# Kernel tuning notes

Hardware: AMD Instinct MI355X
Metric: run time of the kernel (lower is better)

Reference implementation:

```python
import jax, jax.numpy as jnp
import numpy as np

N_NODES = 10000
IN_DIM, EDGE_DIM, HID_DIM, OUT_DIM = 128, 64, 256, 128
N_EDGES = 640000


def setup_inputs() -> dict:
    key = jax.random.key(0)
    ks = jax.random.split(key, 8)
    x = jax.random.normal(ks[0], (N_NODES, IN_DIM), dtype=jnp.float32)
    edge_index = jax.random.randint(ks[1], (2, N_EDGES), 0, N_NODES, dtype=jnp.int64)
    edge_attr = jax.random.normal(ks[2], (N_EDGES, EDGE_DIM), dtype=jnp.float32)
    # MLP params (PyTorch Linear: y = x @ W.T + b), Kaiming-uniform-ish scale
    s1 = 1.0 / np.sqrt(IN_DIM + EDGE_DIM)
    s2 = 1.0 / np.sqrt(HID_DIM)
    W1 = jax.random.uniform(ks[3], (HID_DIM, IN_DIM + EDGE_DIM), minval=-s1, maxval=s1, dtype=jnp.float32)
    b1 = jax.random.uniform(ks[4], (HID_DIM,), minval=-s1, maxval=s1, dtype=jnp.float32)
    W2 = jax.random.uniform(ks[5], (OUT_DIM, HID_DIM), minval=-s2, maxval=s2, dtype=jnp.float32)
    b2 = jax.random.uniform(ks[6], (OUT_DIM,), minval=-s2, maxval=s2, dtype=jnp.float32)
    return {"x": x, "edge_index": edge_index, "edge_attr": edge_attr,
            "W1": W1, "b1": b1, "W2": W2, "b2": b2}


def reference(x, edge_index, edge_attr, W1, b1, W2, b2):
    # GINE-style concat-message conv: gather -> per-edge MLP -> scatter-add.
    src = edge_index[0]  # message source node x_j
    dst = edge_index[1]  # aggregation target node
    m = jnp.concatenate([x[src], edge_attr], axis=-1)         # [E, F+Fe]
    h = jax.nn.relu(m @ W1.T + b1)                            # [E, H]
    msg = h @ W2.T + b2                                       # [E, O]
    out = jax.ops.segment_sum(msg, dst, num_segments=x.shape[0])  # [N, O]
    return out
```

## Files before the change

### kernel.cpp

```cpp
#include <hip/hip_runtime.h>

#define N_NODES 10000
#define IN_DIM 128
#define EDGE_DIM 64
#define HID_DIM 256
#define OUT_DIM 128
#define N_EDGES 640000


typedef __bf16 bf16x8 __attribute__((ext_vector_type(8)));
typedef float f32x4 __attribute__((ext_vector_type(4)));

static __device__ __forceinline__ unsigned pk_pre(float lo, float hi) {
    return (__builtin_bit_cast(unsigned, lo) >> 16) |
           (__builtin_bit_cast(unsigned, hi) & 0xFFFF0000u);
}
static __device__ __forceinline__ unsigned short f2bf(float f) {
    unsigned u = __builtin_bit_cast(unsigned, f);
    u = (u + 0x7fffu + ((u >> 16) & 1u)) >> 16;
    return (unsigned short)u;
}

__global__ void zero_kernel(float* __restrict__ out) {
    int t = blockIdx.x * 256 + threadIdx.x;
    if (t < 320000) ((float4*)out)[t] = make_float4(0.f, 0.f, 0.f, 0.f);
}

#define FENCE_LGKM()  asm volatile("s_waitcnt lgkmcnt(0)" ::: "memory")
#define SCHED_FENCE() __builtin_amdgcn_sched_barrier(0)

__global__ __launch_bounds__(512, 2) void gine_wave2(
    const int* __restrict__ ei,
    const float* __restrict__ x,
    const float* __restrict__ ea,
    const float* __restrict__ W1,
    const float* __restrict__ b1,
    const float* __restrict__ W2,
    const float* __restrict__ b2,
    float* __restrict__ out)
{
    __shared__ __align__(16) unsigned sW1u[128 * 96];
    __shared__ __align__(16) unsigned sW2u[128 * 64];
    __shared__ __align__(16) unsigned sMu[8][16 * 96];

    const int tid  = threadIdx.x;
    const int hb   = blockIdx.x & 1;
    const int bseq = blockIdx.x >> 1;

    for (int i = tid; i < 128 * 96; i += 512) {
        int r = i / 96, c2 = i - r * 96;
        const float* w = W1 + (size_t)(hb * 128 + r) * 192 + c2 * 2;
        sW1u[r * 96 + (c2 ^ ((r & 7) << 2))] = pk_pre(w[0], w[1]);
    }
    for (int i = tid; i < 128 * 64; i += 512) {
        int r = i / 64, c2 = i - r * 64;
        const float* w = W2 + (size_t)r * 256 + hb * 128 + c2 * 2;
        sW2u[r * 64 + (c2 ^ ((r & 7) << 2))] = pk_pre(w[0], w[1]);
    }

    const int lane = tid & 63;
    const int e16  = lane & 15;
    const int q    = lane >> 4;
    const int wv   = tid >> 6;
    const int rsw  = (e16 & 7) << 2;
    unsigned* myM  = &sMu[wv][0];

    f32x4 b1f[8];
    #pragma unroll
    for (int t = 0; t < 8; ++t)
        b1f[t] = *(const f32x4*)(b1 + hb * 128 + t * 16 + q * 4);
    float b2v[8];
    #pragma unroll
    for (int t = 0; t < 8; ++t)
        b2v[t] = hb ? 0.f : b2[t * 16 + e16];

    __syncthreads();

    const int W = bseq * 8 + wv;

    int g = W;
    int sidx = 0, didx = 0;
    if (lane < 16) {
        sidx = ei[g * 16 + lane];
        didx = ei[N_EDGES + g * 16 + lane];
    }
    float4 raw[12];
    #pragma unroll
    for (int j = 0; j < 8; ++j) {
        int ee = 2 * j + (lane >> 5);
        int sr = __shfl(sidx, ee, 64);
        raw[j] = *(const float4*)(x + (size_t)sr * 128 + (lane & 31) * 4);
    }
    #pragma unroll
    for (int j = 0; j < 4; ++j) {
        int ee = 4 * j + (lane >> 4);
        raw[8 + j] = *(const float4*)(ea + (size_t)(g * 16 + ee) * 64 + (lane & 15) * 4);
    }

    for (; g < 40000; g += 2048) {
        const int gn = (g + 2048 < 40000) ? g + 2048 : g;

        int sidx_n = 0, didx_n = 0;
        if (lane < 16) {
            sidx_n = ei[gn * 16 + lane];
            didx_n = ei[N_EDGES + gn * 16 + lane];
        }

        #pragma unroll
        for (int j = 0; j < 8; ++j) {
            int ee = 2 * j + (lane >> 5);
            int c2 = ((lane & 31) * 2) ^ ((ee & 7) << 2);
            uint2 w;
            w.x = pk_pre(raw[j].x, raw[j].y);
            w.y = pk_pre(raw[j].z, raw[j].w);
            *(uint2*)&myM[ee * 96 + c2] = w;
        }
        #pragma unroll
        for (int j = 0; j < 4; ++j) {
            int ee = 4 * j + (lane >> 4);
            int c2 = 64 + (((lane & 15) * 2) ^ ((ee & 7) << 2));
            uint2 w;
            w.x = pk_pre(raw[8 + j].x, raw[8 + j].y);
            w.y = pk_pre(raw[8 + j].z, raw[8 + j].w);
            *(uint2*)&myM[ee * 96 + c2] = w;
        }
        FENCE_LGKM(); SCHED_FENCE();

        f32x4 acc1[8];
        #pragma unroll
        for (int t = 0; t < 8; ++t) acc1[t] = (f32x4){0.f, 0.f, 0.f, 0.f};
        #pragma unroll
        for (int ks = 0; ks < 6; ++ks) {
            const int col = (ks * 16 + q * 4) ^ rsw;
            bf16x8 bfrag = __builtin_bit_cast(bf16x8, *(const int4*)&myM[e16 * 96 + col]);
            #pragma unroll
            for (int mt = 0; mt < 8; ++mt) {
                bf16x8 afrag = __builtin_bit_cast(bf16x8,
                    *(const int4*)&sW1u[(mt * 16 + e16) * 96 + col]);
                acc1[mt] = __builtin_amdgcn_mfma_f32_16x16x32_bf16(afrag, bfrag, acc1[mt], 0, 0, 0);
            }
        }

        unsigned pu0[8], pu1[8];
        #pragma unroll
        for (int mt = 0; mt < 8; ++mt) {
            float v0 = fmaxf(acc1[mt][0] + b1f[mt][0], 0.f);
            float v1 = fmaxf(acc1[mt][1] + b1f[mt][1], 0.f);
            float v2 = fmaxf(acc1[mt][2] + b1f[mt][2], 0.f);
            float v3 = fmaxf(acc1[mt][3] + b1f[mt][3], 0.f);
            pu0[mt] = (unsigned)f2bf(v0) | ((unsigned)f2bf(v1) << 16);
            pu1[mt] = (unsigned)f2bf(v2) | ((unsigned)f2bf(v3) << 16);
        }

        #pragma unroll
        for (int j = 0; j < 8; ++j) {
            int ee = 2 * j + (lane >> 5);
            int sr = __shfl(sidx_n, ee, 64);
            raw[j] = *(const float4*)(x + (size_t)sr * 128 + (lane & 31) * 4);
        }
        #pragma unroll
        for (int j = 0; j < 4; ++j) {
            int ee = 4 * j + (lane >> 4);
            raw[8 + j] = *(const float4*)(ea + (size_t)(gn * 16 + ee) * 64 + (lane & 15) * 4);
        }

        f32x4 acc2[8];
        #pragma unroll
        for (int t = 0; t < 8; ++t) acc2[t] = (f32x4){0.f, 0.f, 0.f, 0.f};
        const int qh = q >> 1;
        const int sa = (q & 1) * 32 + e16;
        #pragma unroll
        for (int kb = 0; kb < 4; ++kb) {
            const int lo0 = (int)pu0[2 * kb],     lo1 = (int)pu1[2 * kb];
            const int hi0 = (int)pu0[2 * kb + 1], hi1 = (int)pu1[2 * kb + 1];
            int4 bi;
            {
                int a0 = __shfl(lo0, sa, 64),      a1 = __shfl(hi0, sa, 64);
                int b0 = __shfl(lo1, sa, 64),      b1_ = __shfl(hi1, sa, 64);
                int c0 = __shfl(lo0, sa + 16, 64), c1 = __shfl(hi0, sa + 16, 64);
                int d0 = __shfl(lo1, sa + 16, 64), d1 = __shfl(hi1, sa + 16, 64);
                bi.x = qh ? a1 : a0;
                bi.y = qh ? b1_ : b0;
                bi.z = qh ? c1 : c0;
                bi.w = qh ? d1 : d0;
            }
            bf16x8 hfrag = __builtin_bit_cast(bf16x8, bi);
            const int col = (kb * 16 + q * 4) ^ rsw;
            #pragma unroll
            for (int ot = 0; ot < 8; ++ot) {
                bf16x8 wfrag = __builtin_bit_cast(bf16x8,
                    *(const int4*)&sW2u[(ot * 16 + e16) * 64 + col]);
                acc2[ot] = __builtin_amdgcn_mfma_f32_16x16x32_bf16(hfrag, wfrag, acc2[ot], 0, 0, 0);
            }
        }

        int dr[4];
        #pragma unroll
        for (int r = 0; r < 4; ++r) dr[r] = __shfl(didx, q * 4 + r, 64);
        #pragma unroll
        for (int r = 0; r < 4; ++r) {
            float* ob = out + (size_t)dr[r] * 128 + e16;
            #pragma unroll
            for (int ot = 0; ot < 8; ++ot)
                unsafeAtomicAdd(ob + ot * 16, acc2[ot][r] + b2v[ot]);
        }

        sidx = sidx_n; didx = didx_n;
    }
}

extern "C" void kernel_launch(void* const* d_in, const int* in_sizes, int n_in,
                              void* d_out, int out_size, void* d_ws, size_t ws_size,
                              hipStream_t stream) {
    const float* x  = (const float*)d_in[0];
    const int*   ei = (const int*)d_in[1];
    const float* ea = (const float*)d_in[2];
    const float* W1 = (const float*)d_in[3];
    const float* b1 = (const float*)d_in[4];
    const float* W2 = (const float*)d_in[5];
    const float* b2 = (const float*)d_in[6];
    float* out = (float*)d_out;

    zero_kernel<<<1250, 256, 0, stream>>>(out);
    gine_wave2<<<512, 512, 0, stream>>>(ei, x, ea, W1, b1, W2, b2, out);
}
```

Before: 722.6 us.

## Compute full hidden dimension per block to halve gathers and atomics

Result: slower. 1.728 ms (+139.2%).

```diff
diff --git a/kernel.cpp b/kernel.cpp
--- a/kernel.cpp
+++ b/kernel.cpp
@@ -20,16 +20,19 @@
     u = (u + 0x7fffu + ((u >> 16) & 1u)) >> 16;
     return (unsigned short)u;
 }
+static __device__ __forceinline__ float bf2f_lo(unsigned u) {
+    return __builtin_bit_cast(float, u << 16);
+}
+static __device__ __forceinline__ float bf2f_hi(unsigned u) {
+    return __builtin_bit_cast(float, u & 0xFFFF0000u);
+}
 
 __global__ void zero_kernel(float* __restrict__ out) {
     int t = blockIdx.x * 256 + threadIdx.x;
     if (t < 320000) ((float4*)out)[t] = make_float4(0.f, 0.f, 0.f, 0.f);
 }
 
-#define FENCE_LGKM()  asm volatile("s_waitcnt lgkmcnt(0)" ::: "memory")
-#define SCHED_FENCE() __builtin_amdgcn_sched_barrier(0)
-
-__global__ __launch_bounds__(512, 2) void gine_wave2(
+__global__ __launch_bounds__(512, 2) void gine_full(
     const int* __restrict__ ei,
     const float* __restrict__ x,
     const float* __restrict__ ea,
@@ -39,23 +42,20 @@
     const float* __restrict__ b2,
     float* __restrict__ out)
 {
-    __shared__ __align__(16) unsigned sW1u[128 * 96];
-    __shared__ __align__(16) unsigned sW2u[128 * 64];
-    __shared__ __align__(16) unsigned sMu[8][16 * 96];
-
-    const int tid  = threadIdx.x;
-    const int hb   = blockIdx.x & 1;
-    const int bseq = blockIdx.x >> 1;
-
-    for (int i = tid; i < 128 * 96; i += 512) {
+    __shared__ __align__(16) unsigned sW1u[256 * 96];
+    __shared__ __align__(16) unsigned sW2u[128 * 128];
+
+    const int tid = threadIdx.x;
+
+    for (int i = tid; i < 256 * 96; i += 512) {
         int r = i / 96, c2 = i - r * 96;
-        const float* w = W1 + (size_t)(hb * 128 + r) * 192 + c2 * 2;
+        const float* w = W1 + (size_t)r * 192 + c2 * 2;
         sW1u[r * 96 + (c2 ^ ((r & 7) << 2))] = pk_pre(w[0], w[1]);
     }
-    for (int i = tid; i < 128 * 64; i += 512) {
-        int r = i / 64, c2 = i - r * 64;
-        const float* w = W2 + (size_t)r * 256 + hb * 128 + c2 * 2;
-        sW2u[r * 64 + (c2 ^ ((r & 7) << 2))] = pk_pre(w[0], w[1]);
+    for (int i = tid; i < 128 * 128; i += 512) {
+        int r = i >> 7, c2 = i & 127;
+        const float* w = W2 + (size_t)r * 256 + c2 * 2;
+        sW2u[r * 128 + (c2 ^ ((r & 7) << 2))] = pk_pre(w[0], w[1]);
     }
 
     const int lane = tid & 63;
@@ -63,20 +63,21 @@
     const int q    = lane >> 4;
     const int wv   = tid >> 6;
     const int rsw  = (e16 & 7) << 2;
-    unsigned* myM  = &sMu[wv][0];
-
-    f32x4 b1f[8];
+
+    unsigned b1p0[16], b1p1[16];
     #pragma unroll
-    for (int t = 0; t < 8; ++t)
-        b1f[t] = *(const f32x4*)(b1 + hb * 128 + t * 16 + q * 4);
+    for (int mt = 0; mt < 16; ++mt) {
+        const float* bp = b1 + mt * 16 + q * 4;
+        b1p0[mt] = pk_pre(bp[0], bp[1]);
+        b1p1[mt] = pk_pre(bp[2], bp[3]);
+    }
     float b2v[8];
     #pragma unroll
-    for (int t = 0; t < 8; ++t)
-        b2v[t] = hb ? 0.f : b2[t * 16 + e16];
+    for (int t = 0; t < 8; ++t) b2v[t] = b2[t * 16 + e16];
 
     __syncthreads();
 
-    const int W = bseq * 8 + wv;
+    const int W = blockIdx.x * 8 + wv;
 
     int g = W;
     int sidx = 0, didx = 0;
@@ -85,16 +86,20 @@
         didx = ei[N_EDGES + g * 16 + lane];
     }
     float4 raw[12];
-    #pragma unroll
-    for (int j = 0; j < 8; ++j) {
-        int ee = 2 * j + (lane >> 5);
-        int sr = __shfl(sidx, ee, 64);
-        raw[j] = *(const float4*)(x + (size_t)sr * 128 + (lane & 31) * 4);
-    }
-    #pragma unroll
-    for (int j = 0; j < 4; ++j) {
-        int ee = 4 * j + (lane >> 4);
-        raw[8 + j] = *(const float4*)(ea + (size_t)(g * 16 + ee) * 64 + (lane & 15) * 4);
+    {
+        const int sr = __shfl(sidx, e16, 64);
+        const float* xr = x + (size_t)sr * 128 + q * 8;
+        #pragma unroll
+        for (int ks = 0; ks < 4; ++ks) {
+            raw[ks * 2 + 0] = *(const float4*)(xr + ks * 32);
+            raw[ks * 2 + 1] = *(const float4*)(xr + ks * 32 + 4);
+        }
+        const float* er = ea + (size_t)(g * 16 + e16) * 64 + q * 8;
+        #pragma unroll
+        for (int t = 0; t < 2; ++t) {
+            raw[8 + t * 2 + 0] = *(const float4*)(er + t * 32);
+            raw[8 + t * 2 + 1] = *(const float4*)(er + t * 32 + 4);
+        }
     }
 
     for (; g < 40000; g += 2048) {
@@ -106,62 +111,51 @@
             didx_n = ei[N_EDGES + gn * 16 + lane];
         }
 
-        #pragma unroll
-        for (int j = 0; j < 8; ++j) {
-            int ee = 2 * j + (lane >> 5);
-            int c2 = ((lane & 31) * 2) ^ ((ee & 7) << 2);
-            uint2 w;
-            w.x = pk_pre(raw[j].x, raw[j].y);
-            w.y = pk_pre(raw[j].z, raw[j].w);
-            *(uint2*)&myM[ee * 96 + c2] = w;
-        }
-        #pragma unroll
-        for (int j = 0; j < 4; ++j) {
-            int ee = 4 * j + (lane >> 4);
-            int c2 = 64 + (((lane & 15) * 2) ^ ((ee & 7) << 2));
-            uint2 w;
-            w.x = pk_pre(raw[8 + j].x, raw[8 + j].y);
-            w.y = pk_pre(raw[8 + j].z, raw[8 + j].w);
-            *(uint2*)&myM[ee * 96 + c2] = w;
-        }
-        FENCE_LGKM(); SCHED_FENCE();
-
-        f32x4 acc1[8];
-        #pragma unroll
-        for (int t = 0; t < 8; ++t) acc1[t] = (f32x4){0.f, 0.f, 0.f, 0.f};
+        f32x4 acc1[16];
+        #pragma unroll
+        for (int t = 0; t < 16; ++t) acc1[t] = (f32x4){0.f, 0.f, 0.f, 0.f};
         #pragma unroll
         for (int ks = 0; ks < 6; ++ks) {
+            int4 bi;
+            bi.x = (int)pk_pre(raw[ks * 2].x, raw[ks * 2].y);
+            bi.y = (int)pk_pre(raw[ks * 2].z, raw[ks * 2].w);
+            bi.z = (int)pk_pre(raw[ks * 2 + 1].x, raw[ks * 2 + 1].y);
+            bi.w = (int)pk_pre(raw[ks * 2 + 1].z, raw[ks * 2 + 1].w);
+            bf16x8 bfrag = __builtin_bit_cast(bf16x8, bi);
             const int col = (ks * 16 + q * 4) ^ rsw;
-            bf16x8 bfrag = __builtin_bit_cast(bf16x8, *(const int4*)&myM[e16 * 96 + col]);
-            #pragma unroll
-            for (int mt = 0; mt < 8; ++mt) {
+            #pragma unroll
+            for (int mt = 0; mt < 16; ++mt) {
                 bf16x8 afrag = __builtin_bit_cast(bf16x8,
                     *(const int4*)&sW1u[(mt * 16 + e16) * 96 + col]);
                 acc1[mt] = __builtin_amdgcn_mfma_f32_16x16x32_bf16(afrag, bfrag, acc1[mt], 0, 0, 0);
             }
         }
 
-        unsigned pu0[8], pu1[8];
-        #pragma unroll
-        for (int mt = 0; mt < 8; ++mt) {
-            float v0 = fmaxf(acc1[mt][0] + b1f[mt][0], 0.f);
-            float v1 = fmaxf(acc1[mt][1] + b1f[mt][1], 0.f);
-            float v2 = fmaxf(acc1[mt][2] + b1f[mt][2], 0.f);
-            float v3 = fmaxf(acc1[mt][3] + b1f[mt][3], 0.f);
+        unsigned pu0[16], pu1[16];
+        #pragma unroll
+        for (int mt = 0; mt < 16; ++mt) {
+            float v0 = fmaxf(acc1[mt][0] + bf2f_lo(b1p0[mt]), 0.f);
+            float v1 = fmaxf(acc1[mt][1] + bf2f_hi(b1p0[mt]), 0.f);
+            float v2 = fmaxf(acc1[mt][2] + bf2f_lo(b1p1[mt]), 0.f);
+            float v3 = fmaxf(acc1[mt][3] + bf2f_hi(b1p1[mt]), 0.f);
             pu0[mt] = (unsigned)f2bf(v0) | ((unsigned)f2bf(v1) << 16);
             pu1[mt] = (unsigned)f2bf(v2) | ((unsigned)f2bf(v3) << 16);
         }
 
-        #pragma unroll
-        for (int j = 0; j < 8; ++j) {
-            int ee = 2 * j + (lane >> 5);
-            int sr = __shfl(sidx_n, ee, 64);
-            raw[j] = *(const float4*)(x + (size_t)sr * 128 + (lane & 31) * 4);
-        }
-        #pragma unroll
-        for (int j = 0; j < 4; ++j) {
-            int ee = 4 * j + (lane >> 4);
-            raw[8 + j] = *(const float4*)(ea + (size_t)(gn * 16 + ee) * 64 + (lane & 15) * 4);
+        {
+            const int sr = __shfl(sidx_n, e16, 64);
+            const float* xr = x + (size_t)sr * 128 + q * 8;
+            #pragma unroll
+            for (int ks = 0; ks < 4; ++ks) {
+                raw[ks * 2 + 0] = *(const float4*)(xr + ks * 32);
+                raw[ks * 2 + 1] = *(const float4*)(xr + ks * 32 + 4);
+            }
+            const float* er = ea + (size_t)(gn * 16 + e16) * 64 + q * 8;
+            #pragma unroll
+            for (int t = 0; t < 2; ++t) {
+                raw[8 + t * 2 + 0] = *(const float4*)(er + t * 32);
+                raw[8 + t * 2 + 1] = *(const float4*)(er + t * 32 + 4);
+            }
         }
 
         f32x4 acc2[8];
@@ -170,7 +164,7 @@
         const int qh = q >> 1;
         const int sa = (q & 1) * 32 + e16;
         #pragma unroll
-        for (int kb = 0; kb < 4; ++kb) {
+        for (int kb = 0; kb < 8; ++kb) {
             const int lo0 = (int)pu0[2 * kb],     lo1 = (int)pu1[2 * kb];
             const int hi0 = (int)pu0[2 * kb + 1], hi1 = (int)pu1[2 * kb + 1];
             int4 bi;
@@ -189,7 +183,7 @@
             #pragma unroll
             for (int ot = 0; ot < 8; ++ot) {
                 bf16x8 wfrag = __builtin_bit_cast(bf16x8,
-                    *(const int4*)&sW2u[(ot * 16 + e16) * 64 + col]);
+                    *(const int4*)&sW2u[(ot * 16 + e16) * 128 + col]);
                 acc2[ot] = __builtin_amdgcn_mfma_f32_16x16x32_bf16(hfrag, wfrag, acc2[ot], 0, 0, 0);
             }
         }
@@ -222,5 +216,5 @@
     float* out = (float*)d_out;
 
     zero_kernel<<<1250, 256, 0, stream>>>(out);
-    gine_wave2<<<512, 512, 0, stream>>>(ei, x, ea, W1, b1, W2, b2, out);
-}
+    gine_full<<<256, 512, 0, stream>>>(ei, x, ea, W1, b1, W2, b2, out);
+}
```
